# Kernel tuning notes

Hardware: AMD Instinct MI355X
Metric: run time of the kernel (lower is better)

The kernel has to match this reference:

```python
import jax, jax.numpy as jnp
import numpy as np

B, S, D = 16, 1024, 768
H = 12
DH = D // H  # 64

def setup_inputs() -> dict:
    key = jax.random.key(0)
    ks = jax.random.split(key, 7)
    scale = 1.0 / np.sqrt(D)
    return {
        "hidden_states": jax.random.normal(ks[0], (B, S, D), dtype=jnp.float32),
        "Wq": jax.random.normal(ks[1], (D, D), dtype=jnp.float32) * scale,
        "bq": jnp.zeros((D,), dtype=jnp.float32),
        "Wk": jax.random.normal(ks[2], (D, D), dtype=jnp.float32) * scale,
        "bk": jnp.zeros((D,), dtype=jnp.float32),
        "Wv": jax.random.normal(ks[3], (D, D), dtype=jnp.float32) * scale,
        "bv": jnp.zeros((D,), dtype=jnp.float32),
    }

def reference(hidden_states, Wq, bq, Wk, bk, Wv, bv):
    # QKV projections: [B,S,D] -> [B,S,H,DH] -> [B,H,S,DH]
    def proj(W, b):
        y = hidden_states @ W.T + b
        return y.reshape(B, S, H, DH).transpose(0, 2, 1, 3)
    q = proj(Wq, bq)
    k = proj(Wk, bk)
    v = proj(Wv, bv)
    # attention scores [B,H,S,S], scaled by sqrt(d_head)
    scores = jnp.einsum('bhqd,bhkd->bhqk', q, k) / jnp.sqrt(jnp.float32(DH))
    probs = jax.nn.softmax(scores, axis=-1)
    # dropout prob = 0.0 (eval) -> identity
    ctx = jnp.einsum('bhqk,bhkd->bhqd', probs, v)
    ctx = ctx.transpose(0, 2, 1, 3).reshape(B, S, D)
    return ctx
```

## Files before the change

### kernel.cpp

```cpp
#include <hip/hip_runtime.h>
#include <hip/hip_bf16.h>

typedef __attribute__((ext_vector_type(8))) short short8;
typedef __attribute__((ext_vector_type(4))) float float4v;
typedef __attribute__((ext_vector_type(2))) unsigned int uint2v;

#define MFMA_BF16 __builtin_amdgcn_mfma_f32_16x16x32_bf16

__device__ __forceinline__ unsigned short f2b(float f) {
  union { float f; unsigned u; } v; v.f = f;
  unsigned r = v.u + 0x7FFFu + ((v.u >> 16) & 1u);
  return (unsigned short)(r >> 16);
}

__device__ __forceinline__ unsigned pk2(float x, float y) {
  float2 v; v.x = x; v.y = y;
  __hip_bfloat162 h = __float22bfloat162_rn(v);
  union { __hip_bfloat162 h; unsigned u; } c; c.h = h;
  return c.u;
}

__device__ __forceinline__ void gld16(const unsigned short* g, unsigned short* l) {
  __builtin_amdgcn_global_load_lds(
      (const __attribute__((address_space(1))) unsigned int*)g,
      (__attribute__((address_space(3))) unsigned int*)l, 16, 0, 0);
}

__device__ __forceinline__ int swa(int r, int k) {
  return (r << 6) + ((((k >> 3) ^ r ^ (r >> 3)) & 7) << 3) + (k & 7);
}

__global__ __launch_bounds__(256) void cast_all(
    const float* __restrict__ hs, const float* __restrict__ Wq,
    const float* __restrict__ Wk, const float* __restrict__ Wv,
    unsigned short* __restrict__ Xb, unsigned short* __restrict__ Wb) {
  const int blk = blockIdx.x;
  const float* src;
  unsigned short* dst;
  int i;
  if (blk < 12288) {
    i = blk * 256 + threadIdx.x;
    src = hs;
    dst = Xb;
  } else {
    const int x = blk - 12288;
    const int z = x / 576;
    i = (x - z * 576) * 256 + threadIdx.x;
    src = (z == 0) ? Wq : (z == 1 ? Wk : Wv);
    dst = Wb + (size_t)z * 589824;
  }
  float4 f = ((const float4*)src)[i];
  uint2 o;
  o.x = pk2(f.x, f.y);
  o.y = pk2(f.z, f.w);
  ((uint2*)dst)[i] = o;
}

__global__ __launch_bounds__(512) void qkv_gemm(
    const unsigned short* __restrict__ X, const unsigned short* __restrict__ Wall,
    const float* __restrict__ b0, const float* __restrict__ b1, const float* __restrict__ b2,
    unsigned short* __restrict__ O0, unsigned short* __restrict__ O1, unsigned short* __restrict__ OVT) {
  extern __shared__ __align__(16) unsigned short LDS[];

  const int g = blockIdx.x;
  const int orig = (g & 7) * 144 + (g >> 3);
  const int mblk = orig / 18;
  const int nblk = orig - mblk * 18;
  const int m0 = mblk * 256, n0p = nblk * 128;

  const int t = threadIdx.x, w = t >> 6, l = t & 63, qd = l >> 4, col = l & 15;
  const int wm64 = (w & 3) * 64, wn64 = (w >> 2) * 64;
  const int qd8 = qd * 8;

  const int cA0 = t, cA1 = 512 + t, cA2 = 1024 + t, cA3 = 1536 + t;
  const int rA0 = cA0 >> 3, rA1 = cA1 >> 3, rA2 = cA2 >> 3, rA3 = cA3 >> 3;
  const int pA0 = (cA0 ^ rA0 ^ (rA0 >> 3)) & 7, pA1 = (cA1 ^ rA1 ^ (rA1 >> 3)) & 7;
  const int pA2 = (cA2 ^ rA2 ^ (rA2 >> 3)) & 7, pA3 = (cA3 ^ rA3 ^ (rA3 >> 3)) & 7;
  const int cB0 = t, cB1 = 512 + t;
  const int rB0 = cB0 >> 3, rB1 = cB1 >> 3;
  const int pB0 = (cB0 ^ rB0 ^ (rB0 >> 3)) & 7, pB1 = (cB1 ^ rB1 ^ (rB1 >> 3)) & 7;

  const unsigned short* Xa0 = X + (size_t)(m0 + rA0) * 768 + pA0 * 8;
  const unsigned short* Xa1 = X + (size_t)(m0 + rA1) * 768 + pA1 * 8;
  const unsigned short* Xa2 = X + (size_t)(m0 + rA2) * 768 + pA2 * 8;
  const unsigned short* Xa3 = X + (size_t)(m0 + rA3) * 768 + pA3 * 8;
  const unsigned short* Wb0 = Wall + (size_t)(n0p + rB0) * 768 + pB0 * 8;
  const unsigned short* Wb1 = Wall + (size_t)(n0p + rB1) * 768 + pB1 * 8;
  const int dA0 = cA0 * 8, dA1 = cA1 * 8, dA2 = cA2 * 8, dA3 = cA3 * 8;
  const int dB0 = cB0 * 8, dB1 = cB1 * 8;

#define STAGE(kt, sb)                                         \
  do {                                                        \
    unsigned short* SA_ = LDS + (sb)*24576;                   \
    unsigned short* SB_ = SA_ + 16384;                        \
    const int kk_ = (kt)*64;                                  \
    gld16(Xa0 + kk_, SA_ + dA0);                              \
    gld16(Xa1 + kk_, SA_ + dA1);                              \
    gld16(Xa2 + kk_, SA_ + dA2);                              \
    gld16(Xa3 + kk_, SA_ + dA3);                              \
    gld16(Wb0 + kk_, SB_ + dB0);                              \
    gld16(Wb1 + kk_, SB_ + dB1);                              \
  } while (0)

  float4v acc[4][4];
#pragma unroll
  for (int i = 0; i < 4; ++i)
#pragma unroll
    for (int j = 0; j < 4; ++j) acc[i][j] = (float4v)0.0f;

#define COMPUTE(cur)                                                          \
  do {                                                                        \
    const unsigned short* Ar_ = LDS + (cur)*24576;                            \
    const unsigned short* Br_ = Ar_ + 16384;                                  \
    _Pragma("unroll") for (int ks = 0; ks < 2; ++ks) {                        \
      short8 af[4], bf[4];                                                    \
      _Pragma("unroll") for (int mi = 0; mi < 4; ++mi)                        \
          af[mi] = *(const short8*)&Ar_[swa(wm64 + mi * 16 + col,             \
                                            ks * 32 + qd8)];                  \
      _Pragma("unroll") for (int ni = 0; ni < 4; ++ni)                        \
          bf[ni] = *(const short8*)&Br_[swa(wn64 + ni * 16 + col,             \
                                            ks * 32 + qd8)];                  \
      __builtin_amdgcn_s_setprio(1);                                          \
      _Pragma("unroll") for (int mi = 0; mi < 4; ++mi)                        \
          _Pragma("unroll") for (int ni = 0; ni < 4; ++ni)                    \
          acc[mi][ni] = MFMA_BF16(af[mi], bf[ni], acc[mi][ni], 0, 0, 0);      \
      __builtin_amdgcn_s_setprio(0);                                          \
    }                                                                         \
  } while (0)

  STAGE(0, 0);
  STAGE(1, 1);
  asm volatile("s_waitcnt vmcnt(6)" ::: "memory");
  __builtin_amdgcn_s_barrier();
  __builtin_amdgcn_sched_barrier(0);

  int cur = 0;
#pragma unroll 1
  for (int kt = 0; kt < 10; ++kt) {
    const int sb = (cur == 0) ? 2 : cur - 1;
    STAGE(kt + 2, sb);
    COMPUTE(cur);
    asm volatile("s_waitcnt vmcnt(6)" ::: "memory");
    __builtin_amdgcn_s_barrier();
    __builtin_amdgcn_sched_barrier(0);
    cur = (cur == 2) ? 0 : cur + 1;
  }
  COMPUTE(cur);
  asm volatile("s_waitcnt vmcnt(0)" ::: "memory");
  __builtin_amdgcn_s_barrier();
  __builtin_amdgcn_sched_barrier(0);
  cur = (cur == 2) ? 0 : cur + 1;
  COMPUTE(cur);

  const int zz = n0p / 768;
  const int nbase = n0p - zz * 768;

  if (zz < 2) {
    unsigned short* O = (zz == 0) ? O0 : O1;
    const float* bias = (zz == 0) ? b0 : b1;
    const float osc = (zz == 0) ? 0.18033688f : 1.0f;
#pragma unroll
    for (int ni = 0; ni < 4; ++ni) {
      const int n = nbase + wn64 + ni * 16 + col;
      const float bb = bias[n];
#pragma unroll
      for (int mi = 0; mi < 4; ++mi)
#pragma unroll
        for (int r = 0; r < 4; ++r) {
          const int m = m0 + wm64 + mi * 16 + qd * 4 + r;
          O[(size_t)m * 768 + n] = f2b((acc[mi][ni][r] + bb) * osc);
        }
    }
  } else {
    __syncthreads();
    unsigned short* T = LDS;
#pragma unroll
    for (int ni = 0; ni < 4; ++ni) {
      const int nl = wn64 + ni * 16 + col;
      const float bb = b2[nbase + nl];
#pragma unroll
      for (int mi = 0; mi < 4; ++mi) {
        const int ml = wm64 + mi * 16 + qd * 4;
        const int mc = ml >> 3;
        ushort4 o;
        o.x = f2b(acc[mi][ni][0] + bb);
        o.y = f2b(acc[mi][ni][1] + bb);
        o.z = f2b(acc[mi][ni][2] + bb);
        o.w = f2b(acc[mi][ni][3] + bb);
        *(ushort4*)&T[(nl << 8) + (((mc ^ (nl & 31)) & 31) << 3) + (ml & 7)] = o;
      }
    }
    __syncthreads();
    const int nl2 = t >> 2;
    const int seg = t & 3;
    const int nglob = nbase + nl2;
    const int hh = nglob >> 6, dd = nglob & 63;
    const int bb2 = m0 >> 10;
    unsigned short* dstp =
        &OVT[(((size_t)bb2 * 12 + hh) * 64 + dd) * 1024 + (m0 & 1023) + seg * 64];
#pragma unroll
    for (int j = 0; j < 8; ++j) {
      const int mc = seg * 8 + j;
      uint4 vv = *(const uint4*)&T[(nl2 << 8) + (((mc ^ (nl2 & 31)) & 31) << 3)];
      *(uint4*)&dstp[j * 8] = vv;
    }
  }
#undef STAGE
#undef COMPUTE
}

__global__ __launch_bounds__(256) void attn(
    const unsigned short* __restrict__ Q, const unsigned short* __restrict__ K,
    const unsigned short* __restrict__ VT, float* __restrict__ O) {
  __shared__ __align__(16) unsigned short Ks0[4096];
  __shared__ __align__(16) unsigned short Ks1[4096];
  __shared__ __align__(16) unsigned short Ks2[4096];
  __shared__ __align__(16) unsigned short Vt0[4096];
  __shared__ __align__(16) unsigned short Vt1[4096];
  __shared__ __align__(16) unsigned short Vt2[4096];

  const int g = blockIdx.x;
  const int orig = (g & 7) * 192 + (g >> 3);
  const int qt = orig & 7;
  const int hb = orig >> 3;
  const int b = hb / 12;
  const int h = hb - b * 12;

  const int t = threadIdx.x, w = t >> 6, l = t & 63, qd = l >> 4, col = l & 15;
  const size_t bh = (size_t)b * 786432 + (size_t)h * 64;
  const unsigned short* Kb = K + bh;
  const unsigned short* VTb = VT + ((size_t)(b * 12 + h)) * 65536;

  short8 qf[2][2];
  {
    const unsigned short* Qg = Q + bh + (size_t)(qt * 128 + w * 32) * 768;
#pragma unroll
    for (int mi = 0; mi < 2; ++mi)
#pragma unroll
      for (int ks = 0; ks < 2; ++ks)
        qf[mi][ks] =
            *(const short8*)&Qg[(size_t)(mi * 16 + col) * 768 + ks * 32 + qd * 8];
  }

  const int c0 = t, c1 = 256 + t;
  const int r0 = c0 >> 3, cc0 = (c0 ^ r0 ^ (r0 >> 3)) & 7;
  const int r1 = c1 >> 3, cc1 = (c1 ^ r1 ^ (r1 >> 3)) & 7;

#define STAGE_K(ktile, dst)                                             \
  do {                                                                  \
    const unsigned short* Kg_ = Kb + (size_t)(ktile)*49152;             \
    gld16(&Kg_[(size_t)r0 * 768 + cc0 * 8], &dst[c0 * 8]);              \
    gld16(&Kg_[(size_t)r1 * 768 + cc1 * 8], &dst[c1 * 8]);              \
  } while (0)

#define STAGE_V(ktile, dst)                                             \
  do {                                                                  \
    const unsigned short* Vg_ = VTb + (ktile)*64;                       \
    gld16(&Vg_[(size_t)r0 * 1024 + cc0 * 8], &dst[c0 * 8]);             \
    gld16(&Vg_[(size_t)r1 * 1024 + cc1 * 8], &dst[c1 * 8]);             \
  } while (0)

  float4v acc[2][4];
  float4v accl[2];
#pragma unroll
  for (int mi = 0; mi < 2; ++mi) {
    accl[mi] = (float4v)0.0f;
#pragma unroll
    for (int dt = 0; dt < 4; ++dt) acc[mi][dt] = (float4v)0.0f;
  }
  float4v sA[2][4], sB[2][4];
  const float4v Zv = (float4v)0.0f;

  short8 ones;
#pragma unroll
  for (int j = 0; j < 8; ++j) ones[j] = (short)0x3F80;

#define QK_TILE(KsR, S)                                                   \
  do {                                                                    \
    short8 kf[2][4];                                                      \
    _Pragma("unroll") for (int ks = 0; ks < 2; ++ks)                      \
        _Pragma("unroll") for (int ni = 0; ni < 4; ++ni)                  \
        kf[ks][ni] =                                                      \
        *(const short8*)&KsR[swa(ni * 16 + col, ks * 32 + qd * 8)];       \
    __builtin_amdgcn_s_setprio(1);                                        \
    _Pragma("unroll") for (int ni = 0; ni < 4; ++ni) {                    \
      S[0][ni] = MFMA_BF16(kf[0][ni], qf[0][0], Zv, 0, 0, 0);             \
      S[1][ni] = MFMA_BF16(kf[0][ni], qf[1][0], Zv, 0, 0, 0);             \
    }                                                                     \
    _Pragma("unroll") for (int ni = 0; ni < 4; ++ni) {                    \
      S[0][ni] = MFMA_BF16(kf[1][ni], qf[0][1], S[0][ni], 0, 0, 0);       \
      S[1][ni] = MFMA_BF16(kf[1][ni], qf[1][1], S[1][ni], 0, 0, 0);       \
    }                                                                     \
    __builtin_amdgcn_s_setprio(0);                                        \
  } while (0)

#define SMPV(S, VtR)                                                      \
  do {                                                                    \
    _Pragma("unroll") for (int s = 0; s < 2; ++s) {                       \
      short8 pf[2];                                                       \
      _Pragma("unroll") for (int mi = 0; mi < 2; ++mi) {                  \
        float4v sa = S[mi][s * 2 + 0];                                    \
        float4v sb = S[mi][s * 2 + 1];                                    \
        unsigned A0 = pk2(__builtin_amdgcn_exp2f(sa[0]),                  \
                          __builtin_amdgcn_exp2f(sa[1]));                 \
        unsigned A1 = pk2(__builtin_amdgcn_exp2f(sa[2]),                  \
                          __builtin_amdgcn_exp2f(sa[3]));                 \
        unsigned B0 = pk2(__builtin_amdgcn_exp2f(sb[0]),                  \
                          __builtin_amdgcn_exp2f(sb[1]));                 \
        unsigned B1 = pk2(__builtin_amdgcn_exp2f(sb[2]),                  \
                          __builtin_amdgcn_exp2f(sb[3]));                 \
        uint2v x0 = __builtin_amdgcn_permlane32_swap(A0, B0, false, false);   \
        uint2v x1 = __builtin_amdgcn_permlane32_swap(A1, B1, false, false);   \
        uint2v y02 = __builtin_amdgcn_permlane16_swap(x0[0], x0[1], false, false); \
        uint2v y13 = __builtin_amdgcn_permlane16_swap(x1[0], x1[1], false, false); \
        union { unsigned u[4]; short8 v; } pu;                            \
        pu.u[0] = y02[0]; pu.u[1] = y13[0];                               \
        pu.u[2] = y02[1]; pu.u[3] = y13[1];                               \
        pf[mi] = pu.v;                                                    \
      }                                                                   \
      const int kk = s * 32 + qd * 8;                                     \
      __builtin_amdgcn_s_setprio(1);                                      \
      _Pragma("unroll") for (int dt = 0; dt < 4; ++dt) {                  \
        short8 vf = *(const short8*)&VtR[swa(dt * 16 + col, kk)];         \
        acc[0][dt] = MFMA_BF16(vf, pf[0], acc[0][dt], 0, 0, 0);           \
        acc[1][dt] = MFMA_BF16(vf, pf[1], acc[1][dt], 0, 0, 0);           \
      }                                                                   \
      accl[0] = MFMA_BF16(ones, pf[0], accl[0], 0, 0, 0);                 \
      accl[1] = MFMA_BF16(ones, pf[1], accl[1], 0, 0, 0);                 \
      __builtin_amdgcn_s_setprio(0);                                      \
    }                                                                     \
  } while (0)

#define W4 asm volatile("s_waitcnt vmcnt(4)" ::: "memory")
#define W2 asm volatile("s_waitcnt vmcnt(2)" ::: "memory")
#define W0 asm volatile("s_waitcnt vmcnt(0)" ::: "memory")
#define BAR                                                               \
  do {                                                                    \
    __builtin_amdgcn_s_barrier();                                         \
    __builtin_amdgcn_sched_barrier(0);                                    \
  } while (0)

#define PIPE(kt, KR, VR, KW, VW, Snew, Sold, WAIT)                        \
  do {                                                                    \
    if ((kt) + 2 < 16) STAGE_K((kt) + 2, KW);                             \
    if ((kt) + 1 < 16) STAGE_V((kt) + 1, VW);                             \
    QK_TILE(KR, Snew);                                                    \
    SMPV(Sold, VR);                                                       \
    WAIT;                                                                 \
    BAR;                                                                  \
  } while (0)

  STAGE_K(0, Ks0);
  STAGE_V(0, Vt0);
  STAGE_K(1, Ks1);
  STAGE_V(1, Vt1);
  STAGE_K(2, Ks2);
  W0;
  BAR;
  QK_TILE(Ks0, sA);
  BAR;

  PIPE(1,  Ks1, Vt0, Ks0, Vt2, sB, sA, W4);
  PIPE(2,  Ks2, Vt1, Ks1, Vt0, sA, sB, W4);
  PIPE(3,  Ks0, Vt2, Ks2, Vt1, sB, sA, W4);
  PIPE(4,  Ks1, Vt0, Ks0, Vt2, sA, sB, W4);
  PIPE(5,  Ks2, Vt1, Ks1, Vt0, sB, sA, W4);
  PIPE(6,  Ks0, Vt2, Ks2, Vt1, sA, sB, W4);
  PIPE(7,  Ks1, Vt0, Ks0, Vt2, sB, sA, W4);
  PIPE(8,  Ks2, Vt1, Ks1, Vt0, sA, sB, W4);
  PIPE(9,  Ks0, Vt2, Ks2, Vt1, sB, sA, W4);
  PIPE(10, Ks1, Vt0, Ks0, Vt2, sA, sB, W4);
  PIPE(11, Ks2, Vt1, Ks1, Vt0, sB, sA, W4);
  PIPE(12, Ks0, Vt2, Ks2, Vt1, sA, sB, W4);
  PIPE(13, Ks1, Vt0, Ks0, Vt2, sB, sA, W4);
  PIPE(14, Ks2, Vt1, Ks0, Vt0, sA, sB, W0);
  QK_TILE(Ks0, sB);
  SMPV(sA, Vt2);
  SMPV(sB, Vt0);

  float* Og = O + (size_t)(b * 1024 + qt * 128) * 768 + h * 64;
#pragma unroll
  for (int mi = 0; mi < 2; ++mi) {
    const float rl = 1.0f / accl[mi][0];
    const int q = w * 32 + mi * 16 + col;
#pragma unroll
    for (int dt = 0; dt < 4; ++dt) {
      float4 o;
      o.x = acc[mi][dt][0] * rl;
      o.y = acc[mi][dt][1] * rl;
      o.z = acc[mi][dt][2] * rl;
      o.w = acc[mi][dt][3] * rl;
      *(float4*)&Og[(size_t)q * 768 + dt * 16 + qd * 4] = o;
    }
  }
#undef STAGE_K
#undef STAGE_V
#undef QK_TILE
#undef SMPV
#undef PIPE
#undef W4
#undef W2
#undef W0
#undef BAR
}

extern "C" void kernel_launch(void* const* d_in, const int* in_sizes, int n_in,
                              void* d_out, int out_size, void* d_ws, size_t ws_size,
                              hipStream_t stream) {
  const float* hs = (const float*)d_in[0];
  const float* Wq = (const float*)d_in[1];
  const float* bq = (const float*)d_in[2];
  const float* Wk = (const float*)d_in[3];
  const float* bk = (const float*)d_in[4];
  const float* Wv = (const float*)d_in[5];
  const float* bv = (const float*)d_in[6];
  float* out = (float*)d_out;
  char* ws = (char*)d_ws;

  unsigned short* Xb = (unsigned short*)ws;
  unsigned short* Wb = (unsigned short*)(ws + 25165824);
  unsigned short* Qb = (unsigned short*)(ws + 28704768);
  unsigned short* Kb = (unsigned short*)(ws + 53870592);
  unsigned short* Vb = (unsigned short*)(ws + 79036416);

  static bool attr_set = false;
  if (!attr_set) {
    hipFuncSetAttribute((const void*)qkv_gemm,
                        hipFuncAttributeMaxDynamicSharedMemorySize, 147456);
    attr_set = true;
  }

  cast_all<<<14016, 256, 0, stream>>>(hs, Wq, Wk, Wv, Xb, Wb);

  qkv_gemm<<<dim3(1152), 512, 147456, stream>>>(Xb, Wb, bq, bk, bv, Qb, Kb, Vb);

  attn<<<dim3(1536), 256, 0, stream>>>(Qb, Kb, Vb, out);
}
```

Measured before the change: 253.8 us.

## Shrink QKV GEMM tile to 128x128 with 256 threads and double buffering

The QKV projection GEMM moves from 256x128 tiles with 512 threads and a 3-stage LDS pipeline to 128x128 tiles with 256 threads and a 2-buffer pipeline. LDS use drops from 144KB to 64KB and the grid doubles to 2304 blocks, so more blocks can be resident per CU and the tail of the launch is finer-grained. The V-transpose epilogue is adapted to the smaller tile. In exchange, each tile reuses operands less, and the wait on all outstanding loads before every barrier exposes more memory latency.

```diff
diff --git a/kernel.cpp b/kernel.cpp
--- a/kernel.cpp
+++ b/kernel.cpp
@@ -56,50 +56,44 @@
   ((uint2*)dst)[i] = o;
 }
 
-__global__ __launch_bounds__(512) void qkv_gemm(
+__global__ __launch_bounds__(256) void qkv_gemm(
     const unsigned short* __restrict__ X, const unsigned short* __restrict__ Wall,
     const float* __restrict__ b0, const float* __restrict__ b1, const float* __restrict__ b2,
     unsigned short* __restrict__ O0, unsigned short* __restrict__ O1, unsigned short* __restrict__ OVT) {
   extern __shared__ __align__(16) unsigned short LDS[];
 
   const int g = blockIdx.x;
-  const int orig = (g & 7) * 144 + (g >> 3);
+  const int orig = (g & 7) * 288 + (g >> 3);
   const int mblk = orig / 18;
   const int nblk = orig - mblk * 18;
-  const int m0 = mblk * 256, n0p = nblk * 128;
+  const int m0 = mblk * 128, n0p = nblk * 128;
 
   const int t = threadIdx.x, w = t >> 6, l = t & 63, qd = l >> 4, col = l & 15;
-  const int wm64 = (w & 3) * 64, wn64 = (w >> 2) * 64;
+  const int wm64 = (w & 1) * 64, wn64 = (w >> 1) * 64;
   const int qd8 = qd * 8;
 
-  const int cA0 = t, cA1 = 512 + t, cA2 = 1024 + t, cA3 = 1536 + t;
-  const int rA0 = cA0 >> 3, rA1 = cA1 >> 3, rA2 = cA2 >> 3, rA3 = cA3 >> 3;
-  const int pA0 = (cA0 ^ rA0 ^ (rA0 >> 3)) & 7, pA1 = (cA1 ^ rA1 ^ (rA1 >> 3)) & 7;
-  const int pA2 = (cA2 ^ rA2 ^ (rA2 >> 3)) & 7, pA3 = (cA3 ^ rA3 ^ (rA3 >> 3)) & 7;
-  const int cB0 = t, cB1 = 512 + t;
-  const int rB0 = cB0 >> 3, rB1 = cB1 >> 3;
-  const int pB0 = (cB0 ^ rB0 ^ (rB0 >> 3)) & 7, pB1 = (cB1 ^ rB1 ^ (rB1 >> 3)) & 7;
-
-  const unsigned short* Xa0 = X + (size_t)(m0 + rA0) * 768 + pA0 * 8;
-  const unsigned short* Xa1 = X + (size_t)(m0 + rA1) * 768 + pA1 * 8;
-  const unsigned short* Xa2 = X + (size_t)(m0 + rA2) * 768 + pA2 * 8;
-  const unsigned short* Xa3 = X + (size_t)(m0 + rA3) * 768 + pA3 * 8;
-  const unsigned short* Wb0 = Wall + (size_t)(n0p + rB0) * 768 + pB0 * 8;
-  const unsigned short* Wb1 = Wall + (size_t)(n0p + rB1) * 768 + pB1 * 8;
-  const int dA0 = cA0 * 8, dA1 = cA1 * 8, dA2 = cA2 * 8, dA3 = cA3 * 8;
-  const int dB0 = cB0 * 8, dB1 = cB1 * 8;
-
-#define STAGE(kt, sb)                                         \
-  do {                                                        \
-    unsigned short* SA_ = LDS + (sb)*24576;                   \
-    unsigned short* SB_ = SA_ + 16384;                        \
-    const int kk_ = (kt)*64;                                  \
-    gld16(Xa0 + kk_, SA_ + dA0);                              \
-    gld16(Xa1 + kk_, SA_ + dA1);                              \
-    gld16(Xa2 + kk_, SA_ + dA2);                              \
-    gld16(Xa3 + kk_, SA_ + dA3);                              \
-    gld16(Wb0 + kk_, SB_ + dB0);                              \
-    gld16(Wb1 + kk_, SB_ + dB1);                              \
+  int rr[4], pp[4];
+#pragma unroll
+  for (int i = 0; i < 4; ++i) {
+    const int c = i * 256 + t;
+    const int r = c >> 3;
+    rr[i] = r;
+    pp[i] = (c ^ r ^ (r >> 3)) & 7;
+  }
+  const unsigned short* Xbase = X + (size_t)m0 * 768;
+  const unsigned short* Wbase = Wall + (size_t)n0p * 768;
+
+#define STAGE(kt, buf)                                                        \
+  do {                                                                        \
+    unsigned short* SA_ = LDS + (buf)*16384;                                  \
+    unsigned short* SB_ = SA_ + 8192;                                         \
+    const int kk_ = (kt)*64;                                                  \
+    _Pragma("unroll") for (int i = 0; i < 4; ++i)                             \
+        gld16(Xbase + (size_t)rr[i] * 768 + kk_ + pp[i] * 8,                  \
+              SA_ + (i * 256 + t) * 8);                                       \
+    _Pragma("unroll") for (int i = 0; i < 4; ++i)                             \
+        gld16(Wbase + (size_t)rr[i] * 768 + kk_ + pp[i] * 8,                  \
+              SB_ + (i * 256 + t) * 8);                                       \
   } while (0)
 
   float4v acc[4][4];
@@ -108,10 +102,10 @@
 #pragma unroll
     for (int j = 0; j < 4; ++j) acc[i][j] = (float4v)0.0f;
 
-#define COMPUTE(cur)                                                          \
+#define COMPUTE(buf)                                                          \
   do {                                                                        \
-    const unsigned short* Ar_ = LDS + (cur)*24576;                            \
-    const unsigned short* Br_ = Ar_ + 16384;                                  \
+    const unsigned short* Ar_ = LDS + (buf)*16384;                            \
+    const unsigned short* Br_ = Ar_ + 8192;                                   \
     _Pragma("unroll") for (int ks = 0; ks < 2; ++ks) {                        \
       short8 af[4], bf[4];                                                    \
       _Pragma("unroll") for (int mi = 0; mi < 4; ++mi)                        \
@@ -129,27 +123,20 @@
   } while (0)
 
   STAGE(0, 0);
-  STAGE(1, 1);
-  asm volatile("s_waitcnt vmcnt(6)" ::: "memory");
-  __builtin_amdgcn_s_barrier();
-  __builtin_amdgcn_sched_barrier(0);
-
-  int cur = 0;
-#pragma unroll 1
-  for (int kt = 0; kt < 10; ++kt) {
-    const int sb = (cur == 0) ? 2 : cur - 1;
-    STAGE(kt + 2, sb);
-    COMPUTE(cur);
-    asm volatile("s_waitcnt vmcnt(6)" ::: "memory");
-    __builtin_amdgcn_s_barrier();
-    __builtin_amdgcn_sched_barrier(0);
-    cur = (cur == 2) ? 0 : cur + 1;
-  }
-  COMPUTE(cur);
   asm volatile("s_waitcnt vmcnt(0)" ::: "memory");
   __builtin_amdgcn_s_barrier();
   __builtin_amdgcn_sched_barrier(0);
-  cur = (cur == 2) ? 0 : cur + 1;
+
+  int cur = 0;
+#pragma unroll 1
+  for (int kt = 0; kt < 11; ++kt) {
+    STAGE(kt + 1, cur ^ 1);
+    COMPUTE(cur);
+    asm volatile("s_waitcnt vmcnt(0)" ::: "memory");
+    __builtin_amdgcn_s_barrier();
+    __builtin_amdgcn_sched_barrier(0);
+    cur ^= 1;
+  }
   COMPUTE(cur);
 
   const int zz = n0p / 768;
@@ -181,27 +168,23 @@
 #pragma unroll
       for (int mi = 0; mi < 4; ++mi) {
         const int ml = wm64 + mi * 16 + qd * 4;
-        const int mc = ml >> 3;
         ushort4 o;
         o.x = f2b(acc[mi][ni][0] + bb);
         o.y = f2b(acc[mi][ni][1] + bb);
         o.z = f2b(acc[mi][ni][2] + bb);
         o.w = f2b(acc[mi][ni][3] + bb);
-        *(ushort4*)&T[(nl << 8) + (((mc ^ (nl & 31)) & 31) << 3) + (ml & 7)] = o;
+        *(ushort4*)&T[(nl << 7) + ((((ml >> 3) ^ nl) & 15) << 3) + (ml & 7)] = o;
       }
     }
     __syncthreads();
-    const int nl2 = t >> 2;
-    const int seg = t & 3;
-    const int nglob = nbase + nl2;
-    const int hh = nglob >> 6, dd = nglob & 63;
-    const int bb2 = m0 >> 10;
+    const int nl = t >> 1, mh = (t & 1) * 64;
+    const int n = nbase + nl, hh = n >> 6, dd = n & 63;
     unsigned short* dstp =
-        &OVT[(((size_t)bb2 * 12 + hh) * 64 + dd) * 1024 + (m0 & 1023) + seg * 64];
+        &OVT[(((size_t)(m0 >> 10) * 12 + hh) * 64 + dd) * 1024 + (m0 & 1023) + mh];
 #pragma unroll
     for (int j = 0; j < 8; ++j) {
-      const int mc = seg * 8 + j;
-      uint4 vv = *(const uint4*)&T[(nl2 << 8) + (((mc ^ (nl2 & 31)) & 31) << 3)];
+      const int mc = (mh >> 3) + j;
+      uint4 vv = *(const uint4*)&T[(nl << 7) + (((mc ^ nl) & 15) << 3)];
       *(uint4*)&dstp[j * 8] = vv;
     }
   }
@@ -332,7 +315,6 @@
   } while (0)
 
 #define W4 asm volatile("s_waitcnt vmcnt(4)" ::: "memory")
-#define W2 asm volatile("s_waitcnt vmcnt(2)" ::: "memory")
 #define W0 asm volatile("s_waitcnt vmcnt(0)" ::: "memory")
 #define BAR                                                               \
   do {                                                                    \
@@ -399,7 +381,6 @@
 #undef SMPV
 #undef PIPE
 #undef W4
-#undef W2
 #undef W0
 #undef BAR
 }
@@ -426,13 +407,13 @@
   static bool attr_set = false;
   if (!attr_set) {
     hipFuncSetAttribute((const void*)qkv_gemm,
-                        hipFuncAttributeMaxDynamicSharedMemorySize, 147456);
+                        hipFuncAttributeMaxDynamicSharedMemorySize, 65536);
     attr_set = true;
   }
 
   cast_all<<<14016, 256, 0, stream>>>(hs, Wq, Wk, Wv, Xb, Wb);
 
-  qkv_gemm<<<dim3(1152), 512, 147456, stream>>>(Xb, Wb, bq, bk, bv, Qb, Kb, Vb);
+  qkv_gemm<<<dim3(2304), 256, 65536, stream>>>(Xb, Wb, bq, bk, bv, Qb, Kb, Vb);
 
   attn<<<dim3(1536), 256, 0, stream>>>(Qb, Kb, Vb, out);
 }
```

Measured after the change: 267.8 us. 1.06x slower.
